# Kernel tuning notes

Hardware: AMD Instinct MI355X
Metric: run time of the kernel (lower is better)

## Reference

```python
import jax, jax.numpy as jnp
import numpy as np

NUM_NODES = 100000
NUM_EDGES = 400000
F_IN = 16          # num_node_features
F_EDGE = 8         # num_edge_features
EMB = 16           # emb_size
NUM_GRAPHS = 256


def setup_inputs() -> dict:
    key = jax.random.key(0)
    ks = jax.random.split(key, 12)
    x = jax.random.normal(ks[0], (NUM_NODES, F_IN), dtype=jnp.float32)
    edge_index = jax.random.randint(ks[1], (2, NUM_EDGES), 0, NUM_NODES, dtype=jnp.int32)
    edge_attr = jax.random.normal(ks[2], (NUM_EDGES, F_EDGE), dtype=jnp.float32)
    batch = jnp.sort(jax.random.randint(ks[3], (NUM_NODES,), 0, NUM_GRAPHS, dtype=jnp.int32))
    s = 0.1
    # edge-network MLP: Linear(F_EDGE -> F_IN*EMB) + ReLU (torch Linear convention: W[out,in])
    nn1_w = jax.random.normal(ks[4], (F_IN * EMB, F_EDGE), dtype=jnp.float32) * s
    nn1_b = jax.random.normal(ks[5], (F_IN * EMB,), dtype=jnp.float32) * s
    # NNConv root weight (bias=False Linear) + separate bias
    root_w = jax.random.normal(ks[6], (EMB, F_IN), dtype=jnp.float32) * s
    conv_b = jax.random.normal(ks[7], (EMB,), dtype=jnp.float32) * s
    lin1_w = jax.random.normal(ks[8], (EMB, 2 * EMB), dtype=jnp.float32) * s
    lin1_b = jax.random.normal(ks[9], (EMB,), dtype=jnp.float32) * s
    lin2_w = jax.random.normal(ks[10], (1, EMB), dtype=jnp.float32) * s
    lin2_b = jax.random.normal(ks[11], (1,), dtype=jnp.float32) * s
    return {"x": x, "edge_index": edge_index, "edge_attr": edge_attr, "batch": batch,
            "nn1_w": nn1_w, "nn1_b": nn1_b, "root_w": root_w, "conv_b": conv_b,
            "lin1_w": lin1_w, "lin1_b": lin1_b, "lin2_w": lin2_w, "lin2_b": lin2_b}


def reference(x, edge_index, edge_attr, batch, nn1_w, nn1_b, root_w, conv_b,
              lin1_w, lin1_b, lin2_w, lin2_b):
    N = x.shape[0]
    src, dst = edge_index[0], edge_index[1]  # PyG: message flows src(j) -> dst(i)
    # edge network -> per-edge weight matrices [E, F_IN, EMB]
    w = jax.nn.relu(edge_attr @ nn1_w.T + nn1_b).reshape(-1, F_IN, EMB)
    # gather source features, per-edge matmul
    msg = jnp.einsum('ei,eio->eo', x[src], w)  # [E, EMB]
    # scatter-mean into target nodes
    sums = jax.ops.segment_sum(msg, dst, num_segments=N)
    cnt = jax.ops.segment_sum(jnp.ones((msg.shape[0],), msg.dtype), dst, num_segments=N)
    agg = sums / jnp.maximum(cnt, 1.0)[:, None]
    # NNConv: root transform + aggregated messages + bias, then outer ReLU
    h = jax.nn.relu(agg + x @ root_w.T + conv_b)  # [N, EMB]
    # global max pool and global mean pool per graph
    gmax = jax.ops.segment_max(h, batch, num_segments=NUM_GRAPHS)
    gsum = jax.ops.segment_sum(h, batch, num_segments=NUM_GRAPHS)
    gcnt = jax.ops.segment_sum(jnp.ones((N,), h.dtype), batch, num_segments=NUM_GRAPHS)
    gmean = gsum / jnp.maximum(gcnt, 1.0)[:, None]
    pooled = jnp.concatenate([gmax, gmean], axis=1)  # [G, 2*EMB]
    h2 = jax.nn.relu(pooled @ lin1_w.T + lin1_b)
    out = h2 @ lin2_w.T + lin2_b  # [G, 1]
    return out
```

## Files before the change

kernel.cpp:

```cpp
#include <hip/hip_runtime.h>

#define NUM_NODES 100000
#define NUM_EDGES 400000
#define F_IN 16
#define F_EDGE 8
#define EMB 16
#define NUM_GRAPHS 256

#define EDGE_TILES 5
#define EDGE_BLOCKS (NUM_EDGES / (32 * EDGE_TILES))


__global__ __launch_bounds__(256) void edge_kernel(
    const float* __restrict__ x, const int* __restrict__ ei,
    const float* __restrict__ ea, const float* __restrict__ nn1_w,
    const float* __restrict__ nn1_b, float* __restrict__ sums,
    float* __restrict__ cnt)
{
    __shared__ float wtp[256 * 12];
    __shared__ float btp[16 * 20];
    __shared__ float xs[32 * 16];
    __shared__ float eas[32 * 8];
    __shared__ int   srcs[32];
    __shared__ int   dsts[32];

    const int tid = threadIdx.x;
    const int eL  = tid >> 4;
    const int o   = tid & 15;

    for (int t = tid; t < F_IN * EMB * F_EDGE; t += 256)
        wtp[(t >> 3) * 12 + (t & 7)] = nn1_w[t];
    btp[(tid & 15) * 20 + (tid >> 4)] = nn1_b[tid];
    __syncthreads();

    float br[F_IN];
    #pragma unroll
    for (int r = 0; r < 4; r++) {
        const float4 b4 = *(const float4*)&btp[o * 20 + 4 * r];
        br[4 * r + 0] = b4.x; br[4 * r + 1] = b4.y;
        br[4 * r + 2] = b4.z; br[4 * r + 3] = b4.w;
    }

    for (int t = 0; t < EDGE_TILES; t++) {
        const int e0 = (blockIdx.x * EDGE_TILES + t) * 32;

        __syncthreads();
        if (tid < 32)      srcs[tid]      = ei[e0 + tid];
        else if (tid < 64) dsts[tid - 32] = ei[NUM_EDGES + e0 + tid - 32];
        eas[tid] = ea[e0 * 8 + tid];
        __syncthreads();
        xs[tid]       = x[srcs[eL]      * 16 + o];
        xs[256 + tid] = x[srcs[16 + eL] * 16 + o];
        __syncthreads();

        const float4 a00 = *(const float4*)&eas[eL * 8];
        const float4 a01 = *(const float4*)&eas[eL * 8 + 4];
        const float4 a10 = *(const float4*)&eas[(16 + eL) * 8];
        const float4 a11 = *(const float4*)&eas[(16 + eL) * 8 + 4];

        float xr0[F_IN], xr1[F_IN];
        #pragma unroll
        for (int r = 0; r < 4; r++) {
            const float4 v0 = *(const float4*)&xs[eL * 16 + 4 * r];
            const float4 v1 = *(const float4*)&xs[(16 + eL) * 16 + 4 * r];
            xr0[4 * r + 0] = v0.x; xr0[4 * r + 1] = v0.y;
            xr0[4 * r + 2] = v0.z; xr0[4 * r + 3] = v0.w;
            xr1[4 * r + 0] = v1.x; xr1[4 * r + 1] = v1.y;
            xr1[4 * r + 2] = v1.z; xr1[4 * r + 3] = v1.w;
        }

        float acc0 = 0.f, acc1 = 0.f;
        #pragma unroll
        for (int i = 0; i < F_IN; i++) {
            const float* wr = &wtp[(i * 16 + o) * 12];
            const float4 w0 = *(const float4*)wr;
            const float4 w1 = *(const float4*)(wr + 4);
            float u = br[i];
            u = fmaf(a00.x, w0.x, u); u = fmaf(a00.y, w0.y, u);
            u = fmaf(a00.z, w0.z, u); u = fmaf(a00.w, w0.w, u);
            u = fmaf(a01.x, w1.x, u); u = fmaf(a01.y, w1.y, u);
            u = fmaf(a01.z, w1.z, u); u = fmaf(a01.w, w1.w, u);
            acc0 = fmaf(xr0[i], fmaxf(u, 0.f), acc0);
            float v = br[i];
            v = fmaf(a10.x, w0.x, v); v = fmaf(a10.y, w0.y, v);
            v = fmaf(a10.z, w0.z, v); v = fmaf(a10.w, w0.w, v);
            v = fmaf(a11.x, w1.x, v); v = fmaf(a11.y, w1.y, v);
            v = fmaf(a11.z, w1.z, v); v = fmaf(a11.w, w1.w, v);
            acc1 = fmaf(xr1[i], fmaxf(v, 0.f), acc1);
        }

        atomicAdd(&sums[dsts[eL] * 16 + o],      acc0);
        atomicAdd(&sums[dsts[16 + eL] * 16 + o], acc1);
        if (o == 0) {
            atomicAdd(&cnt[dsts[eL]],      1.f);
            atomicAdd(&cnt[dsts[16 + eL]], 1.f);
        }
    }
}

__global__ __launch_bounds__(256) void node_kernel(
    const float* __restrict__ x, const int* __restrict__ batch,
    const float* __restrict__ root_w, const float* __restrict__ conv_b,
    const float* __restrict__ sums, const float* __restrict__ cnt,
    unsigned int* __restrict__ gmax, float* __restrict__ gsum,
    float* __restrict__ gcnt)
{
    __shared__ float rwT[256];
    __shared__ float xsh[256];
    __shared__ float ssh[256];
    __shared__ float csh[16];
    __shared__ int   bsh[16];
    __shared__ float hsh[256];

    const int tid = threadIdx.x;
    const int j   = tid >> 4;
    const int o   = tid & 15;
    const int n0  = blockIdx.x * 16;

    rwT[(tid & 15) * 16 + (tid >> 4)] = root_w[tid];
    xsh[tid] = x[n0 * 16 + tid];
    ssh[tid] = sums[n0 * 16 + tid];
    if (tid < 16)      csh[tid]      = cnt[n0 + tid];
    else if (tid < 32) bsh[tid - 16] = batch[n0 + tid - 16];
    __syncthreads();

    float a = conv_b[o] + ssh[j * 16 + o] / fmaxf(csh[j], 1.f);
    #pragma unroll
    for (int i = 0; i < F_IN; i++)
        a = fmaf(xsh[j * 16 + i], rwT[i * 16 + o], a);
    hsh[tid] = fmaxf(a, 0.f);
    __syncthreads();

    if (tid < 16) {
        int cur = bsh[0]; float m = 0.f, s = 0.f;
        for (int jj = 0; jj < 16; jj++) {
            if (bsh[jj] != cur) {
                atomicMax(&gmax[cur * 16 + tid], __float_as_uint(m));
                atomicAdd(&gsum[cur * 16 + tid], s);
                cur = bsh[jj]; m = 0.f; s = 0.f;
            }
            const float h = hsh[jj * 16 + tid];
            m = fmaxf(m, h); s += h;
        }
        atomicMax(&gmax[cur * 16 + tid], __float_as_uint(m));
        atomicAdd(&gsum[cur * 16 + tid], s);
    } else if (tid == 16) {
        int cur = bsh[0]; float c = 0.f;
        for (int jj = 0; jj < 16; jj++) {
            if (bsh[jj] != cur) { atomicAdd(&gcnt[cur], c); cur = bsh[jj]; c = 0.f; }
            c += 1.f;
        }
        atomicAdd(&gcnt[cur], c);
    }
}

__global__ __launch_bounds__(256) void head_kernel(
    const unsigned int* __restrict__ gmax, const float* __restrict__ gsum,
    const float* __restrict__ gcnt,
    const float* __restrict__ lin1_w, const float* __restrict__ lin1_b,
    const float* __restrict__ lin2_w, const float* __restrict__ lin2_b,
    float* __restrict__ out)
{
    const int g = threadIdx.x;

    float pooled[2 * EMB];
    #pragma unroll
    for (int o = 0; o < EMB; o++) pooled[o] = __uint_as_float(gmax[g * 16 + o]);
    const float c = fmaxf(gcnt[g], 1.f);
    #pragma unroll
    for (int o = 0; o < EMB; o++) pooled[EMB + o] = gsum[g * 16 + o] / c;

    float acc = lin2_b[0];
    #pragma unroll
    for (int k = 0; k < EMB; k++) {
        float a = lin1_b[k];
        #pragma unroll
        for (int cc = 0; cc < 2 * EMB; cc++)
            a = fmaf(pooled[cc], lin1_w[k * 32 + cc], a);
        acc = fmaf(fmaxf(a, 0.f), lin2_w[k], acc);
    }
    out[g] = acc;
}

extern "C" void kernel_launch(void* const* d_in, const int* in_sizes, int n_in,
                              void* d_out, int out_size, void* d_ws, size_t ws_size,
                              hipStream_t stream) {
    const float* x      = (const float*)d_in[0];
    const int*   ei     = (const int*)d_in[1];
    const float* ea     = (const float*)d_in[2];
    const int*   batch  = (const int*)d_in[3];
    const float* nn1_w  = (const float*)d_in[4];
    const float* nn1_b  = (const float*)d_in[5];
    const float* root_w = (const float*)d_in[6];
    const float* conv_b = (const float*)d_in[7];
    const float* lin1_w = (const float*)d_in[8];
    const float* lin1_b = (const float*)d_in[9];
    const float* lin2_w = (const float*)d_in[10];
    const float* lin2_b = (const float*)d_in[11];
    float* out = (float*)d_out;

    float*        sums = (float*)d_ws;
    float*        cnt  = sums + (size_t)NUM_NODES * EMB;
    unsigned int* gmax = (unsigned int*)(cnt + NUM_NODES);
    float*        gsum = (float*)(gmax + NUM_GRAPHS * EMB);
    float*        gcnt = gsum + NUM_GRAPHS * EMB;

    const size_t zero_bytes = sizeof(float) *
        ((size_t)NUM_NODES * EMB + NUM_NODES + 2 * NUM_GRAPHS * EMB + NUM_GRAPHS);
    hipMemsetAsync(d_ws, 0, zero_bytes, stream);

    edge_kernel<<<EDGE_BLOCKS, 256, 0, stream>>>(x, ei, ea, nn1_w, nn1_b, sums, cnt);
    node_kernel<<<NUM_NODES / 16, 256, 0, stream>>>(
        x, batch, root_w, conv_b, sums, cnt, gmax, gsum, gcnt);
    head_kernel<<<1, 256, 0, stream>>>(gmax, gsum, gcnt,
                                       lin1_w, lin1_b, lin2_w, lin2_b, out);
}
```

Baseline: 175.8 us.

## Load edge data directly into registers and batch 128 nodes per pooling block

The edge kernel no longer stages src/dst indices, edge attributes and gathered x rows through shared memory. Each thread now loads its own indices, float4 attributes and float4 source rows straight from global memory, which removes three barriers per tile but makes each lane fetch a full 16-float row redundantly. The node kernel now handles 128 nodes per block in 16-node steps and keeps running max/sum/count per graph across steps, so it issues far fewer global atomics for pooling and launches fewer blocks. The trade-off is less parallelism and a longer serial loop per block.

```diff
diff --git a/kernel.cpp b/kernel.cpp
--- a/kernel.cpp
+++ b/kernel.cpp
@@ -9,6 +9,9 @@
 
 #define EDGE_TILES 5
 #define EDGE_BLOCKS (NUM_EDGES / (32 * EDGE_TILES))
+
+#define NPB 128
+#define NODE_BLOCKS ((NUM_NODES + NPB - 1) / NPB)
 
 
 __global__ __launch_bounds__(256) void edge_kernel(
@@ -19,15 +22,12 @@
 {
     __shared__ float wtp[256 * 12];
     __shared__ float btp[16 * 20];
-    __shared__ float xs[32 * 16];
-    __shared__ float eas[32 * 8];
-    __shared__ int   srcs[32];
-    __shared__ int   dsts[32];
 
     const int tid = threadIdx.x;
     const int eL  = tid >> 4;
     const int o   = tid & 15;
 
+    #pragma unroll
     for (int t = tid; t < F_IN * EMB * F_EDGE; t += 256)
         wtp[(t >> 3) * 12 + (t & 7)] = nn1_w[t];
     btp[(tid & 15) * 20 + (tid >> 4)] = nn1_b[tid];
@@ -43,26 +43,24 @@
 
     for (int t = 0; t < EDGE_TILES; t++) {
         const int e0 = (blockIdx.x * EDGE_TILES + t) * 32;
-
-        __syncthreads();
-        if (tid < 32)      srcs[tid]      = ei[e0 + tid];
-        else if (tid < 64) dsts[tid - 32] = ei[NUM_EDGES + e0 + tid - 32];
-        eas[tid] = ea[e0 * 8 + tid];
-        __syncthreads();
-        xs[tid]       = x[srcs[eL]      * 16 + o];
-        xs[256 + tid] = x[srcs[16 + eL] * 16 + o];
-        __syncthreads();
-
-        const float4 a00 = *(const float4*)&eas[eL * 8];
-        const float4 a01 = *(const float4*)&eas[eL * 8 + 4];
-        const float4 a10 = *(const float4*)&eas[(16 + eL) * 8];
-        const float4 a11 = *(const float4*)&eas[(16 + eL) * 8 + 4];
+        const int eA = e0 + eL;
+        const int eB = e0 + 16 + eL;
+
+        const int srcA = ei[eA];
+        const int srcB = ei[eB];
+        const int dstA = ei[NUM_EDGES + eA];
+        const int dstB = ei[NUM_EDGES + eB];
+
+        const float4 a00 = *(const float4*)&ea[eA * 8];
+        const float4 a01 = *(const float4*)&ea[eA * 8 + 4];
+        const float4 a10 = *(const float4*)&ea[eB * 8];
+        const float4 a11 = *(const float4*)&ea[eB * 8 + 4];
 
         float xr0[F_IN], xr1[F_IN];
         #pragma unroll
         for (int r = 0; r < 4; r++) {
-            const float4 v0 = *(const float4*)&xs[eL * 16 + 4 * r];
-            const float4 v1 = *(const float4*)&xs[(16 + eL) * 16 + 4 * r];
+            const float4 v0 = *(const float4*)&x[srcA * 16 + 4 * r];
+            const float4 v1 = *(const float4*)&x[srcB * 16 + 4 * r];
             xr0[4 * r + 0] = v0.x; xr0[4 * r + 1] = v0.y;
             xr0[4 * r + 2] = v0.z; xr0[4 * r + 3] = v0.w;
             xr1[4 * r + 0] = v1.x; xr1[4 * r + 1] = v1.y;
@@ -89,11 +87,11 @@
             acc1 = fmaf(xr1[i], fmaxf(v, 0.f), acc1);
         }
 
-        atomicAdd(&sums[dsts[eL] * 16 + o],      acc0);
-        atomicAdd(&sums[dsts[16 + eL] * 16 + o], acc1);
+        atomicAdd(&sums[dstA * 16 + o], acc0);
+        atomicAdd(&sums[dstB * 16 + o], acc1);
         if (o == 0) {
-            atomicAdd(&cnt[dsts[eL]],      1.f);
-            atomicAdd(&cnt[dsts[16 + eL]], 1.f);
+            atomicAdd(&cnt[dstA], 1.f);
+            atomicAdd(&cnt[dstB], 1.f);
         }
     }
 }
@@ -115,42 +113,58 @@
     const int tid = threadIdx.x;
     const int j   = tid >> 4;
     const int o   = tid & 15;
-    const int n0  = blockIdx.x * 16;
+    const int n0  = blockIdx.x * NPB;
 
     rwT[(tid & 15) * 16 + (tid >> 4)] = root_w[tid];
-    xsh[tid] = x[n0 * 16 + tid];
-    ssh[tid] = sums[n0 * 16 + tid];
-    if (tid < 16)      csh[tid]      = cnt[n0 + tid];
-    else if (tid < 32) bsh[tid - 16] = batch[n0 + tid - 16];
-    __syncthreads();
-
-    float a = conv_b[o] + ssh[j * 16 + o] / fmaxf(csh[j], 1.f);
-    #pragma unroll
-    for (int i = 0; i < F_IN; i++)
-        a = fmaf(xsh[j * 16 + i], rwT[i * 16 + o], a);
-    hsh[tid] = fmaxf(a, 0.f);
-    __syncthreads();
+    const float cb = conv_b[o];
+
+    int   curg = batch[n0];
+    float am = 0.f, asum = 0.f, ac = 0.f;
+
+    for (int s0 = 0; s0 < NPB; s0 += 16) {
+        const int base = n0 + s0;
+        const int idx  = base * 16 + tid;
+        const bool v   = (idx < NUM_NODES * 16);
+        const float xv = v ? x[idx]    : 0.f;
+        const float sv = v ? sums[idx] : 0.f;
+        float cv = 1.f; int bv = -1;
+        if (tid < 16) {
+            const int n = base + tid;
+            if (n < NUM_NODES) { cv = cnt[n]; bv = batch[n]; }
+        }
+        __syncthreads();
+        xsh[tid] = xv; ssh[tid] = sv;
+        if (tid < 16) { csh[tid] = cv; bsh[tid] = bv; }
+        __syncthreads();
+
+        float a = cb + ssh[j * 16 + o] / fmaxf(csh[j], 1.f);
+        #pragma unroll
+        for (int i = 0; i < F_IN; i++)
+            a = fmaf(xsh[j * 16 + i], rwT[i * 16 + o], a);
+        hsh[tid] = fmaxf(a, 0.f);
+        __syncthreads();
+
+        if (tid < 16) {
+            #pragma unroll 1
+            for (int jj = 0; jj < 16; jj++) {
+                const int g = bsh[jj];
+                if (g < 0) break;
+                if (g != curg) {
+                    atomicMax(&gmax[curg * 16 + o], __float_as_uint(am));
+                    atomicAdd(&gsum[curg * 16 + o], asum);
+                    if (o == 0) atomicAdd(&gcnt[curg], ac);
+                    am = 0.f; asum = 0.f; ac = 0.f; curg = g;
+                }
+                const float h = hsh[jj * 16 + o];
+                am = fmaxf(am, h); asum += h; ac += 1.f;
+            }
+        }
+    }
 
     if (tid < 16) {
-        int cur = bsh[0]; float m = 0.f, s = 0.f;
-        for (int jj = 0; jj < 16; jj++) {
-            if (bsh[jj] != cur) {
-                atomicMax(&gmax[cur * 16 + tid], __float_as_uint(m));
-                atomicAdd(&gsum[cur * 16 + tid], s);
-                cur = bsh[jj]; m = 0.f; s = 0.f;
-            }
-            const float h = hsh[jj * 16 + tid];
-            m = fmaxf(m, h); s += h;
-        }
-        atomicMax(&gmax[cur * 16 + tid], __float_as_uint(m));
-        atomicAdd(&gsum[cur * 16 + tid], s);
-    } else if (tid == 16) {
-        int cur = bsh[0]; float c = 0.f;
-        for (int jj = 0; jj < 16; jj++) {
-            if (bsh[jj] != cur) { atomicAdd(&gcnt[cur], c); cur = bsh[jj]; c = 0.f; }
-            c += 1.f;
-        }
-        atomicAdd(&gcnt[cur], c);
+        atomicMax(&gmax[curg * 16 + o], __float_as_uint(am));
+        atomicAdd(&gsum[curg * 16 + o], asum);
+        if (o == 0) atomicAdd(&gcnt[curg], ac);
     }
 }
 
@@ -210,7 +224,7 @@
     hipMemsetAsync(d_ws, 0, zero_bytes, stream);
 
     edge_kernel<<<EDGE_BLOCKS, 256, 0, stream>>>(x, ei, ea, nn1_w, nn1_b, sums, cnt);
-    node_kernel<<<NUM_NODES / 16, 256, 0, stream>>>(
+    node_kernel<<<NODE_BLOCKS, 256, 0, stream>>>(
         x, batch, root_w, conv_b, sums, cnt, gmax, gsum, gcnt);
     head_kernel<<<1, 256, 0, stream>>>(gmax, gsum, gcnt,
                                        lin1_w, lin1_b, lin2_w, lin2_b, out);
```

Result: faster. 165.6 us (-5.8%).
